# Optimization experiments

Hardware: AMD Instinct MI355X
Metric: run time of the kernel (lower is better)

## Reference

```python
import jax, jax.numpy as jnp
import numpy as np

N = 50000; E = 800000; F_IN = 128; E_DIM = 16; HID = 64; HEADS = 2; G = 50; NC = 2
HC1 = HID * HEADS  # 128

def _gatv2(x, edge_attr, src, dst, Wl, bl, Wr, br, We, att, bias, H, C, n):
    # PyG GATv2Conv: x_j -> lin_l, x_i -> lin_r, edge_attr -> lin_edge (no bias)
    xl = (x @ Wl + bl).reshape(n, H, C)
    xr = (x @ Wr + br).reshape(n, H, C)
    e = (edge_attr @ We).reshape(-1, H, C)
    m = jax.nn.leaky_relu(xl[src] + xr[dst] + e, 0.2)   # [E,H,C]
    logits = jnp.einsum('ehc,hc->eh', m, att)           # [E,H]
    # segment softmax over destination nodes (numerically stable)
    mx = jax.ops.segment_max(logits, dst, num_segments=n)
    a = jnp.exp(logits - mx[dst])
    denom = jax.ops.segment_sum(a, dst, num_segments=n)
    alpha = a / (denom[dst] + 1e-16)
    out = jax.ops.segment_sum(xl[src] * alpha[:, :, None], dst, num_segments=n)
    return out.reshape(n, H * C) + bias

def _bn(x, g, b):
    # training-mode batch norm over the node dimension (biased variance)
    mu = x.mean(0)
    var = x.var(0)
    return (x - mu) * jax.lax.rsqrt(var + 1e-5) * g + b

def setup_inputs():
    key = jax.random.key(0)
    k = jax.random.split(key, 24)
    rn = lambda i, shape, s=0.1: jax.random.normal(k[i], shape, dtype=jnp.float32) * s
    return {
        'x': jax.random.normal(k[0], (N, F_IN), dtype=jnp.float32),
        'edge_index': jax.random.randint(k[1], (2, E), 0, N),
        'edge_attr': jax.random.normal(k[2], (E, E_DIM), dtype=jnp.float32),
        'batch': jnp.sort(jax.random.randint(k[3], (N,), 0, G)),
        'skip1_w': rn(4, (F_IN, HC1)), 'skip1_b': rn(5, (HC1,)),
        'c1_wl': rn(6, (F_IN, HC1)), 'c1_bl': rn(7, (HC1,)),
        'c1_wr': rn(8, (F_IN, HC1)), 'c1_br': rn(9, (HC1,)),
        'c1_we': rn(10, (E_DIM, HC1)), 'c1_att': rn(11, (HEADS, HID)), 'c1_bias': rn(12, (HC1,)),
        'bn1_g': jnp.ones((HC1,), jnp.float32), 'bn1_b': jnp.zeros((HC1,), jnp.float32),
        'skip2_w': rn(13, (HC1, HID)), 'skip2_b': rn(14, (HID,)),
        'c2_wl': rn(15, (HC1, HID)), 'c2_bl': rn(16, (HID,)),
        'c2_wr': rn(17, (HC1, HID)), 'c2_br': rn(18, (HID,)),
        'c2_we': rn(19, (E_DIM, HID)), 'c2_att': rn(20, (1, HID)), 'c2_bias': rn(21, (HID,)),
        'bn2_g': jnp.ones((HID,), jnp.float32), 'bn2_b': jnp.zeros((HID,), jnp.float32),
        'cls_w': rn(22, (2 * HID, NC)), 'cls_b': rn(23, (NC,)),
    }

def reference(x, edge_index, edge_attr, batch, skip1_w, skip1_b, c1_wl, c1_bl, c1_wr, c1_br, c1_we, c1_att, c1_bias, bn1_g, bn1_b, skip2_w, skip2_b, c2_wl, c2_bl, c2_wr, c2_br, c2_we, c2_att, c2_bias, bn2_g, bn2_b, cls_w, cls_b):
    src, dst = edge_index[0], edge_index[1]
    xp = x @ skip1_w + skip1_b
    h = _gatv2(x, edge_attr, src, dst, c1_wl, c1_bl, c1_wr, c1_br, c1_we, c1_att, c1_bias, HEADS, HID, N)
    h = jax.nn.elu(_bn(h, bn1_g, bn1_b) + xp)
    xp2 = h @ skip2_w + skip2_b
    h2 = _gatv2(h, edge_attr, src, dst, c2_wl, c2_bl, c2_wr, c2_br, c2_we, c2_att, c2_bias, 1, HID, N)
    h2 = jax.nn.elu(_bn(h2, bn2_g, bn2_b) + xp2)
    counts = jax.ops.segment_sum(jnp.ones((N,), h2.dtype), batch, num_segments=G)
    mean = jax.ops.segment_sum(h2, batch, num_segments=G) / jnp.maximum(counts, 1.0)[:, None]
    mx = jax.ops.segment_max(h2, batch, num_segments=G)
    pooled = jnp.concatenate([mean, mx], axis=1)  # dropout: identity (eval)
    return pooled @ cls_w + cls_b
```

## Files before the change

### kernel.cpp

```cpp
#include <hip/hip_runtime.h>
#include <math.h>

#define NN 50000
#define NE 800000
#define GG 50

typedef unsigned int u32;
typedef unsigned short u16;
typedef float v2f __attribute__((ext_vector_type(2)));
typedef short bf16x8 __attribute__((ext_vector_type(8)));
typedef float f32x4 __attribute__((ext_vector_type(4)));

__device__ __forceinline__ float uaf(u32 x) { return __uint_as_float(x); }

__device__ __forceinline__ u32 bfpack2(float x, float y) {
    u32 a = __float_as_uint(x), b = __float_as_uint(y);
    a = (a + 0x7fffu + ((a >> 16) & 1u)) >> 16;
    b = (b + 0x7fffu + ((b >> 16) & 1u)) & 0xffff0000u;
    return b | a;
}
__device__ __forceinline__ u16 bf16of(float x) {
    u32 a = __float_as_uint(x);
    return (u16)((a + 0x7fffu + ((a >> 16) & 1u)) >> 16);
}

__device__ __forceinline__ u32 fenc(float x) {
    u32 u = __float_as_uint(x);
    return (u >> 31) ? ~u : (u | 0x80000000u);
}
__device__ __forceinline__ float fdec(u32 m) {
    return (m >> 31) ? uaf(m & 0x7fffffffu) : uaf(~m);
}

__device__ __forceinline__ v2f fma2(v2f a, v2f b, v2f c) { return __builtin_elementwise_fma(a, b, c); }
__device__ __forceinline__ v2f max2(v2f a, v2f b) { return __builtin_elementwise_max(a, b); }

template <int CTRL>
__device__ __forceinline__ float dpp_add(float v) {
    int t = __builtin_amdgcn_update_dpp(0, __float_as_int(v), CTRL, 0xf, 0xf, true);
    return v + __int_as_float(t);
}
__device__ __forceinline__ float swz_xor16_add(float v) {
    int t = __builtin_amdgcn_ds_swizzle(__float_as_int(v), 0x401F);
    return v + __int_as_float(t);
}
__device__ __forceinline__ float total64(float v) {
    return __int_as_float(__builtin_amdgcn_readlane(__float_as_int(v), 0))
         + __int_as_float(__builtin_amdgcn_readlane(__float_as_int(v), 32));
}
#define RED4_STAGES(q)  do {                                                    \
    _Pragma("unroll") for (int j = 0; j < 4; ++j) q[j] = dpp_add<0xB1>(q[j]);  \
    _Pragma("unroll") for (int j = 0; j < 4; ++j) q[j] = dpp_add<0x4E>(q[j]);  \
    _Pragma("unroll") for (int j = 0; j < 4; ++j) q[j] = dpp_add<0x141>(q[j]); \
    _Pragma("unroll") for (int j = 0; j < 4; ++j) q[j] = dpp_add<0x140>(q[j]); \
} while (0)

__global__ void zero_u32_kernel(u32* __restrict__ p, int n) {
    int i = blockIdx.x * 256 + threadIdx.x;
    if (i < n) p[i] = 0u;
}

__global__ __launch_bounds__(256) void mega_prep_kernel(
    const int* __restrict__ ei, u32* __restrict__ counts,
    const float* __restrict__ w1a, const float* __restrict__ w1b, const float* __restrict__ w1c,
    u32* __restrict__ WT1,
    const float* __restrict__ w2a, const float* __restrict__ w2b, const float* __restrict__ w2c,
    u32* __restrict__ WT2)
{
    int b = blockIdx.x;
    int t = threadIdx.x;
    if (b < 3125) {
        int e = b * 256 + t;
        if (e < NE) atomicAdd(&counts[ei[NE + e]], 1u);
    } else if (b < 3125 + 96) {
        int i = (b - 3125) * 256 + t;
        const int per = 128 * 64;
        int mat = i / per;
        int r = i - mat * per;
        const float* W = (mat == 0) ? w1a : (mat == 1) ? w1b : w1c;
        int col = r >> 6, c = r & 63;
        WT1[i] = bfpack2(W[(size_t)(2 * c) * 128 + col], W[(size_t)(2 * c + 1) * 128 + col]);
    } else {
        int i = (b - 3221) * 256 + t;
        const int per = 64 * 64;
        int mat = i / per;
        int r = i - mat * per;
        const float* W = (mat == 0) ? w2a : (mat == 1) ? w2b : w2c;
        int col = r >> 6, c = r & 63;
        WT2[i] = bfpack2(W[(size_t)(2 * c) * 64 + col], W[(size_t)(2 * c + 1) * 64 + col]);
    }
}

__global__ __launch_bounds__(256) void scan1_gemm1_kernel(
    const u32* __restrict__ counts, u32* __restrict__ bsums,
    const float* __restrict__ X, const u32* __restrict__ Wt,
    u16* __restrict__ out0, float* __restrict__ out1, float* __restrict__ out2,
    const float* __restrict__ b0, const float* __restrict__ b1, const float* __restrict__ b2,
    int n)
{
    __shared__ __align__(16) u32 SMEM[64 * 68 * 2];
    int t = threadIdx.x;
    if (blockIdx.x < 49) {
        u32* ls = SMEM;
        int base = blockIdx.x * 1024 + t * 4;
        u32 s = 0;
#pragma unroll
        for (int j = 0; j < 4; ++j) { int idx = base + j; if (idx < NN) s += counts[idx]; }
        ls[t] = s;
        __syncthreads();
        for (int off = 128; off > 0; off >>= 1) {
            if (t < off) ls[t] += ls[t + off];
            __syncthreads();
        }
        if (t == 0) bsums[blockIdx.x] = ls[0];
        return;
    }
    u32* Xs = SMEM;
    u32* Ws = SMEM + 64 * 68;
    int row0 = (blockIdx.x - 49) * 64;
#pragma unroll
    for (int i = 0; i < 16; ++i) {
        int flat = t + 256 * i;
        int r = flat >> 6, c = flat & 63;
        int gr = row0 + r;
        u32 v = 0u;
        if (gr < n) {
            float2 f = *(const float2*)(X + (size_t)gr * 128 + c * 2);
            v = bfpack2(f.x, f.y);
        }
        Xs[r * 68 + c] = v;
    }
    int w = t >> 6, lane = t & 63;
    int l15 = lane & 15, quad = lane >> 4;
    for (int nb = 0; nb < 6; ++nb) {
#pragma unroll
        for (int i = 0; i < 16; ++i) {
            int flat = t + 256 * i;
            int cc = flat >> 6, c = flat & 63;
            Ws[cc * 68 + c] = Wt[(size_t)(nb * 64 + cc) * 64 + c];
        }
        __syncthreads();
        f32x4 acc[4] = {};
#pragma unroll
        for (int kk = 0; kk < 4; ++kk) {
            bf16x8 af = *(const bf16x8*)&Xs[(w * 16 + l15) * 68 + kk * 16 + quad * 4];
#pragma unroll
            for (int j = 0; j < 4; ++j) {
                bf16x8 bf = *(const bf16x8*)&Ws[(j * 16 + l15) * 68 + kk * 16 + quad * 4];
                acc[j] = __builtin_amdgcn_mfma_f32_16x16x32_bf16(af, bf, acc[j], 0, 0, 0);
            }
        }
        int mat = nb >> 1;
        int col0 = (nb & 1) * 64;
        const float* bp = (mat == 0) ? b0 : (mat == 1) ? b1 : b2;
#pragma unroll
        for (int j = 0; j < 4; ++j) {
            int col = col0 + j * 16 + l15;
            float bb = bp[col];
#pragma unroll
            for (int r = 0; r < 4; ++r) {
                int grow = row0 + w * 16 + quad * 4 + r;
                if (grow < n) {
                    float v = acc[j][r] + bb;
                    if (mat == 0) out0[(size_t)grow * 128 + col] = bf16of(v);
                    else if (mat == 1) out1[(size_t)grow * 128 + col] = v;
                    else out2[(size_t)grow * 128 + col] = v;
                }
            }
        }
        __syncthreads();
    }
}

__global__ __launch_bounds__(256) void scan_final_kernel(
    const u32* __restrict__ counts, const u32* __restrict__ bsums, int* __restrict__ rowptr)
{
    __shared__ u32 ls[256];
    __shared__ u32 prefsh;
    int t = threadIdx.x;
    if (t < 64) {
        u32 v = (t < 49) ? bsums[t] : 0u;
#pragma unroll
        for (int off = 1; off < 64; off <<= 1) {
            u32 tv = __shfl_up(v, off, 64);
            if (t >= off) v += tv;
        }
        u32 ex = __shfl_up(v, 1, 64);
        if (t == 0) ex = 0u;
        if (t == (int)blockIdx.x) prefsh = ex;
    }
    __syncthreads();
    u32 bpref = prefsh;
    int base = blockIdx.x * 1024 + t * 4;
    u32 c[4];
    u32 s = 0;
#pragma unroll
    for (int j = 0; j < 4; ++j) { int idx = base + j; c[j] = (idx < NN) ? counts[idx] : 0u; s += c[j]; }
    ls[t] = s;
    __syncthreads();
    for (int off = 1; off < 256; off <<= 1) {
        u32 add = (t >= off) ? ls[t - off] : 0u;
        __syncthreads();
        ls[t] += add;
        __syncthreads();
    }
    u32 run = ls[t] - s + bpref;
#pragma unroll
    for (int j = 0; j < 4; ++j) { int idx = base + j; if (idx < NN) { rowptr[idx] = (int)run; } run += c[j]; }
    if (blockIdx.x == 0 && t == 0) rowptr[NN] = NE;
}

__global__ __launch_bounds__(256) void scatter_pack_kernel(
    const int* __restrict__ ei, const float* __restrict__ ea, const int* __restrict__ rowptr,
    u32* __restrict__ cursors, int* __restrict__ srcs, u32* __restrict__ eahs)
{
    int e = blockIdx.x * 256 + threadIdx.x;
    if (e < NE) {
        int sn = ei[e];
        int d = ei[NE + e];
        u32 pos = atomicAdd(&cursors[d], 1u);
        int slot = rowptr[d] + (int)pos;
        srcs[slot] = sn;
        const float4* s4 = (const float4*)(ea + (size_t)e * 16);
        float4 f0 = s4[0], f1 = s4[1], f2 = s4[2], f3 = s4[3];
        uint4 o0 = {bfpack2(f0.x, f0.y), bfpack2(f0.z, f0.w), bfpack2(f1.x, f1.y), bfpack2(f1.z, f1.w)};
        uint4 o1 = {bfpack2(f2.x, f2.y), bfpack2(f2.z, f2.w), bfpack2(f3.x, f3.y), bfpack2(f3.z, f3.w)};
        *(uint4*)(eahs + (size_t)slot * 8) = o0;
        *(uint4*)(eahs + (size_t)slot * 8 + 4) = o1;
    }
}

__global__ __launch_bounds__(256) void gat1_fused_kernel(
    const u32* __restrict__ xlp, const float* __restrict__ xr,
    const u32* __restrict__ eahs, const int* __restrict__ srcs,
    const int* __restrict__ rowptr, const float* __restrict__ We,
    const float* __restrict__ att, const float* __restrict__ bias,
    float* __restrict__ out)
{
    int lane = threadIdx.x & 63;
    int d = (blockIdx.x * 256 + threadIdx.x) >> 6;
    if (d >= NN) return;
    int du = __builtin_amdgcn_readfirstlane(d);
    int beg = rowptr[du], end = rowptr[du + 1];
    int c0 = lane * 2;
    v2f w[16];
#pragma unroll
    for (int k = 0; k < 16; ++k) {
        float2 t2 = *(const float2*)(We + k * 128 + c0);
        w[k] = (v2f){t2.x, t2.y};
    }
    float a0 = att[c0], a1 = att[c0 + 1];
    float2 bt = *(const float2*)(bias + c0);
    float2 xq = *(const float2*)(xr + (size_t)du * 128 + c0);
    v2f xrv = {xq.x, xq.y};

    float s = 0.f;
    v2f acc = {0.f, 0.f};

    int i = beg;
    for (; i + 4 <= end; i += 4) {
        float q[4]; v2f xv[4];
#pragma unroll
        for (int j = 0; j < 4; ++j) {
            const u32* er = eahs + (size_t)(i + j) * 8;
            int sn = srcs[i + j];
            u32 px = xlp[(size_t)sn * 64 + lane];
            v2f e = {0.f, 0.f};
#pragma unroll
            for (int kk = 0; kk < 8; ++kk) {
                u32 pk = er[kk];
                float s1 = uaf(pk << 16), s2 = uaf(pk & 0xffff0000u);
                e = fma2(w[2 * kk],     (v2f){s1, s1}, e);
                e = fma2(w[2 * kk + 1], (v2f){s2, s2}, e);
            }
            xv[j] = (v2f){uaf(px << 16), uaf(px & 0xffff0000u)};
            v2f mm = xv[j] + xrv + e;
            v2f lk = max2(mm, mm * 0.2f);
            q[j] = fmaf(lk.x, a0, lk.y * a1);
        }
        RED4_STAGES(q);
#pragma unroll
        for (int j = 0; j < 4; ++j) q[j] = swz_xor16_add(q[j]);
        float w0 = __expf(q[0]), w1 = __expf(q[1]);
        float w2 = __expf(q[2]), w3 = __expf(q[3]);
        s += (w0 + w1) + (w2 + w3);
        acc = fma2(xv[0], (v2f){w0, w0}, acc);
        acc = fma2(xv[1], (v2f){w1, w1}, acc);
        acc = fma2(xv[2], (v2f){w2, w2}, acc);
        acc = fma2(xv[3], (v2f){w3, w3}, acc);
    }
    for (; i < end; ++i) {
        const u32* er = eahs + (size_t)i * 8;
        int sn = srcs[i];
        u32 px = xlp[(size_t)sn * 64 + lane];
        v2f e = {0.f, 0.f};
#pragma unroll
        for (int kk = 0; kk < 8; ++kk) {
            u32 pk = er[kk];
            float s1 = uaf(pk << 16), s2 = uaf(pk & 0xffff0000u);
            e = fma2(w[2 * kk],     (v2f){s1, s1}, e);
            e = fma2(w[2 * kk + 1], (v2f){s2, s2}, e);
        }
        v2f xv = {uaf(px << 16), uaf(px & 0xffff0000u)};
        v2f mm = xv + xrv + e;
        v2f lk = max2(mm, mm * 0.2f);
        float p = fmaf(lk.x, a0, lk.y * a1);
        p = dpp_add<0xB1>(p);
        p = dpp_add<0x4E>(p);
        p = dpp_add<0x141>(p);
        p = dpp_add<0x140>(p);
        p = swz_xor16_add(p);
        float ww = __expf(p);
        s += ww;
        acc = fma2(xv, (v2f){ww, ww}, acc);
    }
    float inv = 1.f / (s + 1e-16f);
    float2 o;
    o.x = fmaf(acc.x, inv, bt.x);
    o.y = fmaf(acc.y, inv, bt.y);
    *(float2*)(out + (size_t)d * 128 + c0) = o;
}

__global__ __launch_bounds__(256) void gat2_fused_kernel(
    const u16* __restrict__ xlp, const float* __restrict__ xr,
    const u32* __restrict__ eahs, const int* __restrict__ srcs,
    const int* __restrict__ rowptr, const float* __restrict__ We,
    const float* __restrict__ att, const float* __restrict__ bias,
    float* __restrict__ out)
{
    int lane = threadIdx.x & 63;
    int d = (blockIdx.x * 256 + threadIdx.x) >> 6;
    if (d >= NN) return;
    int du = __builtin_amdgcn_readfirstlane(d);
    int beg = rowptr[du], end = rowptr[du + 1];
    float w[16];
#pragma unroll
    for (int k = 0; k < 16; ++k) w[k] = We[k * 64 + lane];
    float a0 = att[lane];
    float bb = bias[lane];
    float xrv = xr[(size_t)du * 64 + lane];

    float s = 0.f, acc = 0.f;

    int i = beg;
    for (; i + 4 <= end; i += 4) {
        float q[4]; float xv[4];
#pragma unroll
        for (int j = 0; j < 4; ++j) {
            const u32* er = eahs + (size_t)(i + j) * 8;
            int sn = srcs[i + j];
            xv[j] = uaf((u32)xlp[(size_t)sn * 64 + lane] << 16);
            float e = 0.f;
#pragma unroll
            for (int kk = 0; kk < 8; ++kk) {
                u32 pk = er[kk];
                float s1 = uaf(pk << 16), s2 = uaf(pk & 0xffff0000u);
                e = fmaf(s1, w[2 * kk], e);
                e = fmaf(s2, w[2 * kk + 1], e);
            }
            float mm = xv[j] + xrv + e;
            mm = fmaxf(mm, 0.2f * mm);
            q[j] = mm * a0;
        }
        RED4_STAGES(q);
#pragma unroll
        for (int j = 0; j < 4; ++j) { q[j] = swz_xor16_add(q[j]); q[j] = total64(q[j]); }
        float w0 = __expf(q[0]), w1 = __expf(q[1]);
        float w2 = __expf(q[2]), w3 = __expf(q[3]);
        s += (w0 + w1) + (w2 + w3);
        acc += fmaf(w0, xv[0], fmaf(w1, xv[1], fmaf(w2, xv[2], w3 * xv[3])));
    }
    for (; i < end; ++i) {
        const u32* er = eahs + (size_t)i * 8;
        int sn = srcs[i];
        float xv = uaf((u32)xlp[(size_t)sn * 64 + lane] << 16);
        float e = 0.f;
#pragma unroll
        for (int kk = 0; kk < 8; ++kk) {
            u32 pk = er[kk];
            float s1 = uaf(pk << 16), s2 = uaf(pk & 0xffff0000u);
            e = fmaf(s1, w[2 * kk], e);
            e = fmaf(s2, w[2 * kk + 1], e);
        }
        float mm = xv + xrv + e;
        mm = fmaxf(mm, 0.2f * mm);
        float p = mm * a0;
        p = dpp_add<0xB1>(p);
        p = dpp_add<0x4E>(p);
        p = dpp_add<0x141>(p);
        p = dpp_add<0x140>(p);
        p = swz_xor16_add(p);
        p = total64(p);
        float ww = __expf(p);
        s += ww;
        acc = fmaf(ww, xv, acc);
    }
    out[(size_t)d * 64 + lane] = acc / (s + 1e-16f) + bb;
}

__global__ __launch_bounds__(256) void gemm2_fused_kernel(
    const float* __restrict__ H, const float* __restrict__ XPin,
    const float* __restrict__ stats, const float* __restrict__ bg, const float* __restrict__ bbv,
    const u32* __restrict__ Wt,
    u16* __restrict__ out0, float* __restrict__ out1, float* __restrict__ out2,
    const float* __restrict__ b0, const float* __restrict__ b1, const float* __restrict__ b2,
    int n)
{
    __shared__ __align__(16) u32 Xs[64 * 68];
    __shared__ __align__(16) u32 Ws[64 * 68];
    int t = threadIdx.x;
    int row0 = blockIdx.x * 64;
    int c = t & 63;
    int ch0 = 2 * c, ch1 = ch0 + 1;
    float mu0 = stats[ch0] * (1.f / NN), mu1 = stats[ch1] * (1.f / NN);
    float var0 = stats[128 + ch0] * (1.f / NN) - mu0 * mu0;
    float var1 = stats[128 + ch1] * (1.f / NN) - mu1 * mu1;
    float s0 = rsqrtf(var0 + 1e-5f) * bg[ch0];
    float s1 = rsqrtf(var1 + 1e-5f) * bg[ch1];
    float t0 = bbv[ch0] - mu0 * s0;
    float t1 = bbv[ch1] - mu1 * s1;
#pragma unroll
    for (int i = 0; i < 16; ++i) {
        int flat = t + 256 * i;
        int r = flat >> 6;
        int gr = row0 + r;
        u32 v = 0u;
        if (gr < n) {
            float2 hv = *(const float2*)(H + (size_t)gr * 128 + ch0);
            float2 xv = *(const float2*)(XPin + (size_t)gr * 128 + ch0);
            float v0 = fmaf(hv.x, s0, t0) + xv.x;
            float v1 = fmaf(hv.y, s1, t1) + xv.y;
            v0 = (v0 > 0.f) ? v0 : expm1f(v0);
            v1 = (v1 > 0.f) ? v1 : expm1f(v1);
            v = bfpack2(v0, v1);
        }
        Xs[r * 68 + c] = v;
    }
    int w = t >> 6, lane = t & 63;
    int l15 = lane & 15, quad = lane >> 4;
    for (int nb = 0; nb < 3; ++nb) {
#pragma unroll
        for (int i = 0; i < 16; ++i) {
            int flat = t + 256 * i;
            int cc = flat >> 6, cw = flat & 63;
            Ws[cc * 68 + cw] = Wt[(size_t)(nb * 64 + cc) * 64 + cw];
        }
        __syncthreads();
        f32x4 acc[4] = {};
#pragma unroll
        for (int kk = 0; kk < 4; ++kk) {
            bf16x8 af = *(const bf16x8*)&Xs[(w * 16 + l15) * 68 + kk * 16 + quad * 4];
#pragma unroll
            for (int j = 0; j < 4; ++j) {
                bf16x8 bf = *(const bf16x8*)&Ws[(j * 16 + l15) * 68 + kk * 16 + quad * 4];
                acc[j] = __builtin_amdgcn_mfma_f32_16x16x32_bf16(af, bf, acc[j], 0, 0, 0);
            }
        }
        const float* bp = (nb == 0) ? b0 : (nb == 1) ? b1 : b2;
#pragma unroll
        for (int j = 0; j < 4; ++j) {
            int col = j * 16 + l15;
            float bb = bp[col];
#pragma unroll
            for (int r = 0; r < 4; ++r) {
                int grow = row0 + w * 16 + quad * 4 + r;
                if (grow < n) {
                    float v = acc[j][r] + bb;
                    if (nb == 0) out0[(size_t)grow * 64 + col] = bf16of(v);
                    else if (nb == 1) out1[(size_t)grow * 64 + col] = v;
                    else out2[(size_t)grow * 64 + col] = v;
                }
            }
        }
        __syncthreads();
    }
}

template <int C>
__global__ __launch_bounds__(256) void bn_stats_kernel(const float* __restrict__ h, float* __restrict__ stats) {
    const int SUB = 256 / C;
    int t = threadIdx.x;
    int c = t & (C - 1);
    int rs = t / C;
    int r0 = blockIdx.x * 512;
    int r1 = min(NN, r0 + 512);
    float s = 0.f, s2 = 0.f;
    for (int r = r0 + rs; r < r1; r += SUB) {
        float v = h[(size_t)r * C + c];
        s += v; s2 = fmaf(v, v, s2);
    }
    __shared__ float ls[256], ls2[256];
    ls[t] = s; ls2[t] = s2;
    __syncthreads();
    if (rs == 0) {
        for (int j = 1; j < SUB; ++j) { s += ls[j * C + c]; s2 += ls2[j * C + c]; }
        atomicAdd(&stats[c], s);
        atomicAdd(&stats[C + c], s2);
    }
}

__global__ __launch_bounds__(256) void pool_acc_kernel(
    const float* __restrict__ D, const float* __restrict__ xp2,
    const float* __restrict__ stats, const float* __restrict__ bg, const float* __restrict__ bbv,
    const int* __restrict__ batch,
    float* __restrict__ psum, u32* __restrict__ pmax)
{
    int t = threadIdx.x;
    int lane = t & 63, rs = t >> 6;
    float mu = stats[lane] * (1.f / NN);
    float var = stats[64 + lane] * (1.f / NN) - mu * mu;
    float sc = rsqrtf(var + 1e-5f) * bg[lane];
    float tb = bbv[lane] - mu * sc;
    int r0 = blockIdx.x * 128;
    int r1 = min(NN, r0 + 128);
    int curg = -1;
    float sum = 0.f, mx = -INFINITY;
    for (int r = r0 + rs; r < r1; r += 4) {
        int g = batch[r];
        if (g != curg) {
            if (curg >= 0) {
                atomicAdd(&psum[curg * 64 + lane], sum);
                atomicMax(&pmax[curg * 64 + lane], fenc(mx));
            }
            curg = g; sum = 0.f; mx = -INFINITY;
        }
        float v = fmaf(D[(size_t)r * 64 + lane], sc, tb) + xp2[(size_t)r * 64 + lane];
        v = (v > 0.f) ? v : expm1f(v);
        sum += v; mx = fmaxf(mx, v);
    }
    if (curg >= 0) {
        atomicAdd(&psum[curg * 64 + lane], sum);
        atomicMax(&pmax[curg * 64 + lane], fenc(mx));
    }
}

__global__ __launch_bounds__(64) void pool_fin_kernel(
    const float* __restrict__ psum, const u32* __restrict__ pmax,
    const int* __restrict__ batch,
    const float* __restrict__ cw, const float* __restrict__ cb,
    float* __restrict__ outp)
{
    int g = blockIdx.x;
    int lane = threadIdx.x;
    int lo = 0, hi = NN;
    while (lo < hi) { int mid = (lo + hi) >> 1; if (batch[mid] < g) lo = mid + 1; else hi = mid; }
    int s0 = lo;
    hi = NN;
    while (lo < hi) { int mid = (lo + hi) >> 1; if (batch[mid] < g + 1) lo = mid + 1; else hi = mid; }
    int e0 = lo;
    float cnt = (float)(e0 - s0);
    float mean = psum[g * 64 + lane] / fmaxf(cnt, 1.f);
    float mx = fdec(pmax[g * 64 + lane]);
#pragma unroll
    for (int c = 0; c < 2; ++c) {
        float v = fmaf(mean, cw[lane * 2 + c], mx * cw[(64 + lane) * 2 + c]);
        v = dpp_add<0xB1>(v);
        v = dpp_add<0x4E>(v);
        v = dpp_add<0x141>(v);
        v = dpp_add<0x140>(v);
        v = swz_xor16_add(v);
        v = total64(v);
        if (lane == 0) outp[g * 2 + c] = v + cb[c];
    }
}

extern "C" void kernel_launch(void* const* d_in, const int* in_sizes, int n_in,
                              void* d_out, int out_size, void* d_ws, size_t ws_size,
                              hipStream_t stream)
{
    const float* x       = (const float*)d_in[0];
    const int*   ei      = (const int*)d_in[1];
    const float* ea      = (const float*)d_in[2];
    const int*   batch   = (const int*)d_in[3];
    const float* skip1_w = (const float*)d_in[4];
    const float* skip1_b = (const float*)d_in[5];
    const float* c1_wl   = (const float*)d_in[6];
    const float* c1_bl   = (const float*)d_in[7];
    const float* c1_wr   = (const float*)d_in[8];
    const float* c1_br   = (const float*)d_in[9];
    const float* c1_we   = (const float*)d_in[10];
    const float* c1_att  = (const float*)d_in[11];
    const float* c1_bias = (const float*)d_in[12];
    const float* bn1_g   = (const float*)d_in[13];
    const float* bn1_b   = (const float*)d_in[14];
    const float* skip2_w = (const float*)d_in[15];
    const float* skip2_b = (const float*)d_in[16];
    const float* c2_wl   = (const float*)d_in[17];
    const float* c2_bl   = (const float*)d_in[18];
    const float* c2_wr   = (const float*)d_in[19];
    const float* c2_br   = (const float*)d_in[20];
    const float* c2_we   = (const float*)d_in[21];
    const float* c2_att  = (const float*)d_in[22];
    const float* c2_bias = (const float*)d_in[23];
    const float* bn2_g   = (const float*)d_in[24];
    const float* bn2_b   = (const float*)d_in[25];
    const float* cls_w   = (const float*)d_in[26];
    const float* cls_b   = (const float*)d_in[27];
    float* outp = (float*)d_out;

    float* ws = (float*)d_ws;
    size_t o = 0;
    float* A   = ws + o; o += 6400000;
    float* B   = ws + o; o += 6400000;
    float* Cb  = ws + o; o += 6400000;
    float* D   = ws + o; o += 6400000;
    int*   SRCS  = (int*)(ws + o); o += 800000;
    u32*   EAHS  = (u32*)(ws + o); o += 6400000;
    u32*   XPx   = (u32*)(ws + o); o += 3200000;
    u32*   WT1   = (u32*)(ws + o); o += 24576;
    u32*   WT2   = (u32*)(ws + o); o += 12288;
    u32*   COUNTS  = (u32*)(ws + o); o += 50000;
    u32*   CURSORS = (u32*)(ws + o); o += 50000;
    float* STATS1  = ws + o; o += 256;
    float* STATS2  = ws + o; o += 128;
    float* PSUM    = ws + o; o += 3200;
    u32*   PMAX    = (u32*)(ws + o); o += 3200;
    int*   ROWPTR  = (int*)(ws + o); o += 50016;
    u32*   BSUMS   = (u32*)(ws + o); o += 64;

    u16*   XL1P = (u16*)A;
    u16*   XL2P = (u16*)A;
    float* xr2  = A + 3200000;
    float* xp2  = (float*)XPx;

    zero_u32_kernel<<<(106784 + 255) / 256, 256, 0, stream>>>(COUNTS, 106784);
    mega_prep_kernel<<<3269, 256, 0, stream>>>(ei, COUNTS,
        c1_wl, c1_wr, skip1_w, WT1, c2_wl, c2_wr, skip2_w, WT2);
    scan1_gemm1_kernel<<<831, 256, 0, stream>>>(COUNTS, BSUMS, x, WT1,
        XL1P, B, Cb, c1_bl, c1_br, skip1_b, NN);
    scan_final_kernel<<<49, 256, 0, stream>>>(COUNTS, BSUMS, ROWPTR);
    scatter_pack_kernel<<<3125, 256, 0, stream>>>(ei, ea, ROWPTR, CURSORS, SRCS, EAHS);

    gat1_fused_kernel<<<NN / 4, 256, 0, stream>>>((const u32*)XL1P, B, EAHS, SRCS, ROWPTR,
        c1_we, c1_att, c1_bias, D);
    bn_stats_kernel<128><<<98, 256, 0, stream>>>(D, STATS1);

    gemm2_fused_kernel<<<782, 256, 0, stream>>>(D, Cb, STATS1, bn1_g, bn1_b, WT2,
        XL2P, xr2, xp2, c2_bl, c2_br, skip2_b, NN);
    gat2_fused_kernel<<<NN / 4, 256, 0, stream>>>(XL2P, xr2, EAHS, SRCS, ROWPTR,
        c2_we, c2_att, c2_bias, D);
    bn_stats_kernel<64><<<98, 256, 0, stream>>>(D, STATS2);

    pool_acc_kernel<<<(NN + 127) / 128, 256, 0, stream>>>(D, xp2, STATS2, bn2_g, bn2_b,
        batch, PSUM, PMAX);
    pool_fin_kernel<<<GG, 64, 0, stream>>>(PSUM, PMAX, batch, cls_w, cls_b, outp);
}
```

Baseline: 552.7 us.

## Software-pipeline edge gathers in GAT aggregation kernels with double-buffered registers

New measurement: 545.7 us. No clear change (-1.3%).

```diff
diff --git a/kernel.cpp b/kernel.cpp
--- a/kernel.cpp
+++ b/kernel.cpp
@@ -249,7 +249,7 @@
         float2 t2 = *(const float2*)(We + k * 128 + c0);
         w[k] = (v2f){t2.x, t2.y};
     }
-    float a0 = att[c0], a1 = att[c0 + 1];
+    float at0 = att[c0], at1 = att[c0 + 1];
     float2 bt = *(const float2*)(bias + c0);
     float2 xq = *(const float2*)(xr + (size_t)du * 128 + c0);
     v2f xrv = {xq.x, xq.y};
@@ -257,40 +257,72 @@
     float s = 0.f;
     v2f acc = {0.f, 0.f};
 
-    int i = beg;
-    for (; i + 4 <= end; i += 4) {
-        float q[4]; v2f xv[4];
-#pragma unroll
-        for (int j = 0; j < 4; ++j) {
-            const u32* er = eahs + (size_t)(i + j) * 8;
-            int sn = srcs[i + j];
-            u32 px = xlp[(size_t)sn * 64 + lane];
-            v2f e = {0.f, 0.f};
-#pragma unroll
-            for (int kk = 0; kk < 8; ++kk) {
-                u32 pk = er[kk];
-                float s1 = uaf(pk << 16), s2 = uaf(pk & 0xffff0000u);
-                e = fma2(w[2 * kk],     (v2f){s1, s1}, e);
-                e = fma2(w[2 * kk + 1], (v2f){s2, s2}, e);
-            }
-            xv[j] = (v2f){uaf(px << 16), uaf(px & 0xffff0000u)};
-            v2f mm = xv[j] + xrv + e;
-            v2f lk = max2(mm, mm * 0.2f);
-            q[j] = fmaf(lk.x, a0, lk.y * a1);
-        }
-        RED4_STAGES(q);
-#pragma unroll
-        for (int j = 0; j < 4; ++j) q[j] = swz_xor16_add(q[j]);
-        float w0 = __expf(q[0]), w1 = __expf(q[1]);
-        float w2 = __expf(q[2]), w3 = __expf(q[3]);
-        s += (w0 + w1) + (w2 + w3);
-        acc = fma2(xv[0], (v2f){w0, w0}, acc);
-        acc = fma2(xv[1], (v2f){w1, w1}, acc);
-        acc = fma2(xv[2], (v2f){w2, w2}, acc);
-        acc = fma2(xv[3], (v2f){w3, w3}, acc);
-    }
-    for (; i < end; ++i) {
-        const u32* er = eahs + (size_t)i * 8;
+    int cnt = (end - beg) >> 2;
+    int sA[4]; uint4 eA0[4], eA1[4]; u32 xA[4];
+    int sB[4]; uint4 eB0[4], eB1[4]; u32 xB[4];
+
+#define G1_LOAD(SN, E0, E1, X, base_) do {                                     \
+    _Pragma("unroll")                                                          \
+    for (int j = 0; j < 4; ++j) SN[j] = srcs[(base_) + j];                     \
+    _Pragma("unroll")                                                          \
+    for (int j = 0; j < 4; ++j) {                                              \
+        const uint4* e4_ = (const uint4*)(eahs + (size_t)((base_) + j) * 8);   \
+        E0[j] = e4_[0]; E1[j] = e4_[1];                                        \
+    }                                                                          \
+    _Pragma("unroll")                                                          \
+    for (int j = 0; j < 4; ++j) X[j] = xlp[(size_t)SN[j] * 64 + lane];         \
+    __builtin_amdgcn_sched_barrier(0);                                         \
+} while (0)
+
+#define G1_PROC(E0, E1, X) do {                                                \
+    float q[4]; v2f xv[4];                                                     \
+    _Pragma("unroll")                                                          \
+    for (int j = 0; j < 4; ++j) {                                              \
+        u32 ew[8] = {E0[j].x, E0[j].y, E0[j].z, E0[j].w,                       \
+                     E1[j].x, E1[j].y, E1[j].z, E1[j].w};                      \
+        v2f e = {0.f, 0.f};                                                    \
+        _Pragma("unroll")                                                      \
+        for (int kk = 0; kk < 8; ++kk) {                                       \
+            u32 pk = ew[kk];                                                   \
+            float s1 = uaf(pk << 16), s2 = uaf(pk & 0xffff0000u);              \
+            e = fma2(w[2 * kk],     (v2f){s1, s1}, e);                         \
+            e = fma2(w[2 * kk + 1], (v2f){s2, s2}, e);                         \
+        }                                                                      \
+        u32 pxv = X[j];                                                        \
+        xv[j] = (v2f){uaf(pxv << 16), uaf(pxv & 0xffff0000u)};                 \
+        v2f mm = xv[j] + xrv + e;                                              \
+        v2f lk = max2(mm, mm * 0.2f);                                          \
+        q[j] = fmaf(lk.x, at0, lk.y * at1);                                    \
+    }                                                                          \
+    RED4_STAGES(q);                                                            \
+    _Pragma("unroll")                                                          \
+    for (int j = 0; j < 4; ++j) q[j] = swz_xor16_add(q[j]);                    \
+    float w0 = __expf(q[0]), w1 = __expf(q[1]);                                \
+    float w2 = __expf(q[2]), w3 = __expf(q[3]);                                \
+    s += (w0 + w1) + (w2 + w3);                                                \
+    acc = fma2(xv[0], (v2f){w0, w0}, acc);                                     \
+    acc = fma2(xv[1], (v2f){w1, w1}, acc);                                     \
+    acc = fma2(xv[2], (v2f){w2, w2}, acc);                                     \
+    acc = fma2(xv[3], (v2f){w3, w3}, acc);                                     \
+} while (0)
+
+    if (cnt > 0) {
+        G1_LOAD(sA, eA0, eA1, xA, beg);
+        int g = 0;
+        for (; g + 2 <= cnt; g += 2) {
+            G1_LOAD(sB, eB0, eB1, xB, beg + (g + 1) * 4);
+            G1_PROC(eA0, eA1, xA);
+            if (g + 2 < cnt) G1_LOAD(sA, eA0, eA1, xA, beg + (g + 2) * 4);
+            G1_PROC(eB0, eB1, xB);
+        }
+        if (g < cnt) G1_PROC(eA0, eA1, xA);
+    }
+#undef G1_LOAD
+#undef G1_PROC
+    for (int i = beg + cnt * 4; i < end; ++i) {
+        const uint4* e4 = (const uint4*)(eahs + (size_t)i * 8);
+        uint4 ql = e4[0], qh = e4[1];
+        u32 er[8] = {ql.x, ql.y, ql.z, ql.w, qh.x, qh.y, qh.z, qh.w};
         int sn = srcs[i];
         u32 px = xlp[(size_t)sn * 64 + lane];
         v2f e = {0.f, 0.f};
@@ -304,7 +336,7 @@
         v2f xv = {uaf(px << 16), uaf(px & 0xffff0000u)};
         v2f mm = xv + xrv + e;
         v2f lk = max2(mm, mm * 0.2f);
-        float p = fmaf(lk.x, a0, lk.y * a1);
+        float p = fmaf(lk.x, at0, lk.y * at1);
         p = dpp_add<0xB1>(p);
         p = dpp_add<0x4E>(p);
         p = dpp_add<0x141>(p);
@@ -336,42 +368,74 @@
     float w[16];
 #pragma unroll
     for (int k = 0; k < 16; ++k) w[k] = We[k * 64 + lane];
-    float a0 = att[lane];
+    float at0 = att[lane];
     float bb = bias[lane];
     float xrv = xr[(size_t)du * 64 + lane];
 
     float s = 0.f, acc = 0.f;
 
-    int i = beg;
-    for (; i + 4 <= end; i += 4) {
-        float q[4]; float xv[4];
-#pragma unroll
-        for (int j = 0; j < 4; ++j) {
-            const u32* er = eahs + (size_t)(i + j) * 8;
-            int sn = srcs[i + j];
-            xv[j] = uaf((u32)xlp[(size_t)sn * 64 + lane] << 16);
-            float e = 0.f;
-#pragma unroll
-            for (int kk = 0; kk < 8; ++kk) {
-                u32 pk = er[kk];
-                float s1 = uaf(pk << 16), s2 = uaf(pk & 0xffff0000u);
-                e = fmaf(s1, w[2 * kk], e);
-                e = fmaf(s2, w[2 * kk + 1], e);
-            }
-            float mm = xv[j] + xrv + e;
-            mm = fmaxf(mm, 0.2f * mm);
-            q[j] = mm * a0;
-        }
-        RED4_STAGES(q);
-#pragma unroll
-        for (int j = 0; j < 4; ++j) { q[j] = swz_xor16_add(q[j]); q[j] = total64(q[j]); }
-        float w0 = __expf(q[0]), w1 = __expf(q[1]);
-        float w2 = __expf(q[2]), w3 = __expf(q[3]);
-        s += (w0 + w1) + (w2 + w3);
-        acc += fmaf(w0, xv[0], fmaf(w1, xv[1], fmaf(w2, xv[2], w3 * xv[3])));
-    }
-    for (; i < end; ++i) {
-        const u32* er = eahs + (size_t)i * 8;
+    int cnt = (end - beg) >> 2;
+    int sA[4]; uint4 eA0[4], eA1[4]; float xA[4];
+    int sB[4]; uint4 eB0[4], eB1[4]; float xB[4];
+
+#define G2_LOAD(SN, E0, E1, X, base_) do {                                     \
+    _Pragma("unroll")                                                          \
+    for (int j = 0; j < 4; ++j) SN[j] = srcs[(base_) + j];                     \
+    _Pragma("unroll")                                                          \
+    for (int j = 0; j < 4; ++j) {                                              \
+        const uint4* e4_ = (const uint4*)(eahs + (size_t)((base_) + j) * 8);   \
+        E0[j] = e4_[0]; E1[j] = e4_[1];                                        \
+    }                                                                          \
+    _Pragma("unroll")                                                          \
+    for (int j = 0; j < 4; ++j)                                                \
+        X[j] = uaf((u32)xlp[(size_t)SN[j] * 64 + lane] << 16);                 \
+    __builtin_amdgcn_sched_barrier(0);                                         \
+} while (0)
+
+#define G2_PROC(E0, E1, X) do {                                                \
+    float q[4];                                                                \
+    _Pragma("unroll")                                                          \
+    for (int j = 0; j < 4; ++j) {                                              \
+        u32 ew[8] = {E0[j].x, E0[j].y, E0[j].z, E0[j].w,                       \
+                     E1[j].x, E1[j].y, E1[j].z, E1[j].w};                      \
+        float e = 0.f;                                                         \
+        _Pragma("unroll")                                                      \
+        for (int kk = 0; kk < 8; ++kk) {                                       \
+            u32 pk = ew[kk];                                                   \
+            float s1 = uaf(pk << 16), s2 = uaf(pk & 0xffff0000u);              \
+            e = fmaf(s1, w[2 * kk], e);                                        \
+            e = fmaf(s2, w[2 * kk + 1], e);                                    \
+        }                                                                      \
+        float mm = X[j] + xrv + e;                                             \
+        mm = fmaxf(mm, 0.2f * mm);                                             \
+        q[j] = mm * at0;                                                       \
+    }                                                                          \
+    RED4_STAGES(q);                                                            \
+    _Pragma("unroll")                                                          \
+    for (int j = 0; j < 4; ++j) { q[j] = swz_xor16_add(q[j]); q[j] = total64(q[j]); } \
+    float w0 = __expf(q[0]), w1 = __expf(q[1]);                                \
+    float w2 = __expf(q[2]), w3 = __expf(q[3]);                                \
+    s += (w0 + w1) + (w2 + w3);                                                \
+    acc += fmaf(w0, X[0], fmaf(w1, X[1], fmaf(w2, X[2], w3 * X[3])));          \
+} while (0)
+
+    if (cnt > 0) {
+        G2_LOAD(sA, eA0, eA1, xA, beg);
+        int g = 0;
+        for (; g + 2 <= cnt; g += 2) {
+            G2_LOAD(sB, eB0, eB1, xB, beg + (g + 1) * 4);
+            G2_PROC(eA0, eA1, xA);
+            if (g + 2 < cnt) G2_LOAD(sA, eA0, eA1, xA, beg + (g + 2) * 4);
+            G2_PROC(eB0, eB1, xB);
+        }
+        if (g < cnt) G2_PROC(eA0, eA1, xA);
+    }
+#undef G2_LOAD
+#undef G2_PROC
+    for (int i = beg + cnt * 4; i < end; ++i) {
+        const uint4* e4 = (const uint4*)(eahs + (size_t)i * 8);
+        uint4 ql = e4[0], qh = e4[1];
+        u32 er[8] = {ql.x, ql.y, ql.z, ql.w, qh.x, qh.y, qh.z, qh.w};
         int sn = srcs[i];
         float xv = uaf((u32)xlp[(size_t)sn * 64 + lane] << 16);
         float e = 0.f;
@@ -384,7 +448,7 @@
         }
         float mm = xv + xrv + e;
         mm = fmaxf(mm, 0.2f * mm);
-        float p = mm * a0;
+        float p = mm * at0;
         p = dpp_add<0xB1>(p);
         p = dpp_add<0x4E>(p);
         p = dpp_add<0x141>(p);
```
